# Optimization experiments

Measured on AMD Instinct MI355X. Metric: run time of the kernel, lower is better.

Reference implementation:

```python
import jax, jax.numpy as jnp
import numpy as np

B, D, L, H = 2048, 64, 64, 512  # batch, in_dim, latent_space, hidden


def setup_inputs() -> dict:
    key = jax.random.key(0)
    ks = jax.random.split(key, 12)
    inp = {
        "x": jax.random.normal(ks[0], (B, D), jnp.float32),
        "koopman": jax.random.normal(ks[1], (B, L, D), jnp.float32),
    }
    dims = [(L, H), (H, H), (H, H), (H, D)]
    k = 2
    for pfx in ("s", "t"):
        for j, (fi, fo) in enumerate(dims):
            inp[f"{pfx}W{j+1}"] = jax.random.normal(ks[k], (fi, fo), jnp.float32) / np.sqrt(fi).astype(np.float32)
            inp[f"{pfx}b{j+1}"] = jnp.zeros((fo,), jnp.float32)
            k += 1
    return inp


def _mlp(z, W1, b1, W2, b2, W3, b3, W4, b4):
    h = jnp.tanh(z @ W1 + b1)
    h = jnp.tanh(h @ W2 + b2)
    h = jnp.tanh(h @ W3 + b3)
    return h @ W4 + b4


def reference(x, koopman,
              sW1, sb1, sW2, sb2, sW3, sb3, sW4, sb4,
              tW1, tb1, tW2, tb2, tW3, tb3, tW4, tb4):
    # koopman: (B, L, D) -> z: (B, D, L); column i of the torch loop is z[:, i, :]
    z = jnp.swapaxes(koopman, 1, 2)
    s = _mlp(z, sW1, sb1, sW2, sb2, sW3, sb3, sW4, sb4)  # (B, D, D)
    t = _mlp(z, tW1, tb1, tW2, tb2, tW3, tb3, tW4, tb4)  # (B, D, D)
    # loop kept only output column i for input column i -> diagonal over last two dims
    ds = jnp.diagonal(s, axis1=1, axis2=2)  # (B, D)
    dt = jnp.diagonal(t, axis1=1, axis2=2)  # (B, D)
    return (x - dt) * jnp.exp(-ds)
```

## Files before the change

kernel.cpp:

```cpp
#include <hip/hip_runtime.h>


typedef _Float16 f16;
typedef _Float16 f16x8 __attribute__((ext_vector_type(8)));
typedef float f32x4 __attribute__((ext_vector_type(4)));

#define WPACK_PER_NET 589824
#define OFF_W1 0
#define OFF_W2 32768
#define OFF_W3 294912
#define OFF_W4T 557056
#define WPACK_BYTES (2u * WPACK_PER_NET * sizeof(f16))

__global__ void pack_weights(const float* __restrict__ sW1, const float* __restrict__ sW2,
                             const float* __restrict__ sW3, const float* __restrict__ sW4,
                             const float* __restrict__ tW1, const float* __restrict__ tW2,
                             const float* __restrict__ tW3, const float* __restrict__ tW4,
                             f16* __restrict__ dst) {
  int idx = blockIdx.x * 256 + threadIdx.x;
  if (idx >= 2 * WPACK_PER_NET) return;
  int net = idx >= WPACK_PER_NET;
  int f = idx - net * WPACK_PER_NET;
  const float* W1 = net ? tW1 : sW1;
  const float* W2 = net ? tW2 : sW2;
  const float* W3 = net ? tW3 : sW3;
  const float* W4 = net ? tW4 : sW4;
  float v;
  if (f < OFF_W2) {
    int j = f & 7, lane = (f >> 3) & 63, nt = (f >> 9) & 31, kk = f >> 14;
    v = W1[(kk * 32 + (lane >> 4) * 8 + j) * 512 + nt * 16 + (lane & 15)];
  } else if (f < OFF_W3) {
    int f2 = f - OFF_W2;
    int j = f2 & 7, lane = (f2 >> 3) & 63, nt = (f2 >> 9) & 31, kk = f2 >> 14;
    v = W2[(kk * 32 + (lane >> 4) * 8 + j) * 512 + nt * 16 + (lane & 15)];
  } else if (f < OFF_W4T) {
    int f3 = f - OFF_W3;
    int j = f3 & 7, lane = (f3 >> 3) & 63, nt = (f3 >> 9) & 31, kk = f3 >> 14;
    v = W3[(kk * 32 + (lane >> 4) * 8 + j) * 512 + nt * 16 + (lane & 15)];
  } else {
    int f4 = f - OFF_W4T;
    v = W4[(f4 & 511) * 64 + (f4 >> 9)];
  }
  dst[net * WPACK_PER_NET + f] = (f16)v;
}

__device__ __forceinline__ int aidx(int m, int k) {
  return (((k >> 5) * 4 + (m >> 4)) * 64 + (m & 15) + ((k >> 3) & 3) * 16) * 8 + (k & 7);
}

__device__ __forceinline__ float fast_tanh(float x) {
  float e = __expf(x + x);
  return fmaf(-2.0f, __builtin_amdgcn_rcpf(e + 1.0f), 1.0f);
}

template <bool PACKED>
__device__ __forceinline__ void load_b(const f16* __restrict__ Wblk,
                                       const float* __restrict__ Wraw,
                                       int kk, int wave, int lane, f16x8* bdst) {
  if (PACKED) {
#pragma unroll
    for (int nt = 0; nt < 4; nt++)
      bdst[nt] = *(const f16x8*)(Wblk + kk * 16384 + ((wave * 4 + nt) * 64 + lane) * 8);
  } else {
    int n0 = wave * 64 + (lane & 15);
    int kb = kk * 32 + (lane >> 4) * 8;
#pragma unroll
    for (int nt = 0; nt < 4; nt++) {
      f16x8 v;
#pragma unroll
      for (int j = 0; j < 8; j++) v[j] = (f16)Wraw[(kb + j) * 512 + n0 + nt * 16];
      bdst[nt] = v;
    }
  }
}

template <int NS, bool PACKED>
__device__ __forceinline__ void mlp_layer(const f16* __restrict__ Wblk,
                                          const float* __restrict__ Wraw,
                                          const float* __restrict__ bias,
                                          const f16* Asrc, f16* Hout,
                                          int wave, int lane, int sbase) {
  f32x4 acc[4][4];
#pragma unroll
  for (int nt = 0; nt < 4; nt++) {
    float bv = bias[wave * 64 + nt * 16 + (lane & 15)];
#pragma unroll
    for (int mt = 0; mt < 4; mt++) acc[mt][nt] = f32x4{bv, bv, bv, bv};
  }

  f16x8 bb[2][4];
  load_b<PACKED>(Wblk, Wraw, 0, wave, lane, bb[0]);
#pragma unroll
  for (int kk = 0; kk < NS; kk++) {
    if (kk + 1 < NS) load_b<PACKED>(Wblk, Wraw, kk + 1, wave, lane, bb[(kk + 1) & 1]);
    const f16* ab = Asrc + kk * 2048 + lane * 8;
    f16x8 a[4];
#pragma unroll
    for (int mt = 0; mt < 4; mt++) a[mt] = *(const f16x8*)(ab + mt * 512);
#pragma unroll
    for (int mt = 0; mt < 4; mt++)
#pragma unroll
      for (int nt = 0; nt < 4; nt++)
        acc[mt][nt] = __builtin_amdgcn_mfma_f32_16x16x32_f16(a[mt], bb[kk & 1][nt],
                                                             acc[mt][nt], 0, 0, 0);
  }
  __syncthreads();

  f16* hb = Hout + sbase;
#pragma unroll
  for (int mt = 0; mt < 4; mt++)
#pragma unroll
    for (int nt = 0; nt < 4; nt++)
#pragma unroll
      for (int r = 0; r < 4; r++)
        hb[(nt >> 1) * 2048 + mt * 512 + (nt & 1) * 256 + r * 8] =
            (f16)fast_tanh(acc[mt][nt][r]);
  __syncthreads();
}

template <bool PACKED>
__global__ __launch_bounds__(512, 4) void decoder_main(
    const float* __restrict__ x, const float* __restrict__ koop,
    const f16* __restrict__ wpack,
    const float* __restrict__ sW1, const float* __restrict__ sW2,
    const float* __restrict__ sW3, const float* __restrict__ sW4,
    const float* __restrict__ tW1, const float* __restrict__ tW2,
    const float* __restrict__ tW3, const float* __restrict__ tW4,
    const float* __restrict__ sb1, const float* __restrict__ sb2,
    const float* __restrict__ sb3, const float* __restrict__ sb4,
    const float* __restrict__ tb1, const float* __restrict__ tb2,
    const float* __restrict__ tb3, const float* __restrict__ tb4,
    float* __restrict__ out) {
  __shared__ __align__(16) f16 ZA[4096];
  __shared__ __align__(16) f16 HA[32768];
  __shared__ float redBuf[2][64];

  const int b = blockIdx.x;
  const int t = threadIdx.x;
  const int wave = t >> 6, lane = t & 63;
  const int sbase =
      wave * 4096 + (lane >> 4) * 32 + ((lane & 15) >> 3) * 128 + (lane & 7);

  const float* kb = koop + b * 4096;
#pragma unroll
  for (int i = 0; i < 8; i++) {
    int flat = t + 512 * i;
    ZA[aidx(flat & 63, flat >> 6)] = (f16)kb[flat];
  }
  __syncthreads();

  for (int net = 0; net < 2; net++) {
    const f16* wb = PACKED ? (wpack + net * WPACK_PER_NET) : (const f16*)0;
    const float* W1 = net ? tW1 : sW1;
    const float* W2 = net ? tW2 : sW2;
    const float* W3 = net ? tW3 : sW3;
    const float* W4 = net ? tW4 : sW4;
    const float* b1 = net ? tb1 : sb1;
    const float* b2 = net ? tb2 : sb2;
    const float* b3 = net ? tb3 : sb3;
    const float* b4 = net ? tb4 : sb4;
    mlp_layer<2, PACKED>(PACKED ? wb + OFF_W1 : 0, W1, b1, ZA, HA, wave, lane, sbase);
    mlp_layer<16, PACKED>(PACKED ? wb + OFF_W2 : 0, W2, b2, HA, HA, wave, lane, sbase);
    mlp_layer<16, PACKED>(PACKED ? wb + OFF_W3 : 0, W3, b3, HA, HA, wave, lane, sbase);

    int i = t >> 3, sub = t & 7;
    float p = 0.f;
#pragma unroll
    for (int q = 0; q < 8; q++) {
      int k0 = sub * 64 + q * 8;
      f16x8 hv = *(const f16x8*)&HA[aidx(i, k0)];
      if (PACKED) {
        f16x8 wv = *(const f16x8*)&wb[OFF_W4T + i * 512 + k0];
#pragma unroll
        for (int j = 0; j < 8; j++) p += (float)hv[j] * (float)wv[j];
      } else {
#pragma unroll
        for (int j = 0; j < 8; j++) p += (float)hv[j] * W4[(k0 + j) * 64 + i];
      }
    }
    p += __shfl_down(p, 4, 8);
    p += __shfl_down(p, 2, 8);
    p += __shfl_down(p, 1, 8);
    if (sub == 0) redBuf[net][i] = p + b4[i];
    __syncthreads();
  }

  if (t < 64) {
    out[b * 64 + t] = (x[b * 64 + t] - redBuf[1][t]) * __expf(-redBuf[0][t]);
  }
}

extern "C" void kernel_launch(void* const* d_in, const int* in_sizes, int n_in,
                              void* d_out, int out_size, void* d_ws, size_t ws_size,
                              hipStream_t stream) {
  const float* x    = (const float*)d_in[0];
  const float* koop = (const float*)d_in[1];
  const float* sW1 = (const float*)d_in[2];  const float* sb1 = (const float*)d_in[3];
  const float* sW2 = (const float*)d_in[4];  const float* sb2 = (const float*)d_in[5];
  const float* sW3 = (const float*)d_in[6];  const float* sb3 = (const float*)d_in[7];
  const float* sW4 = (const float*)d_in[8];  const float* sb4 = (const float*)d_in[9];
  const float* tW1 = (const float*)d_in[10]; const float* tb1 = (const float*)d_in[11];
  const float* tW2 = (const float*)d_in[12]; const float* tb2 = (const float*)d_in[13];
  const float* tW3 = (const float*)d_in[14]; const float* tb3 = (const float*)d_in[15];
  const float* tW4 = (const float*)d_in[16]; const float* tb4 = (const float*)d_in[17];
  float* out = (float*)d_out;

  if (ws_size >= (size_t)WPACK_BYTES) {
    f16* wpack = (f16*)d_ws;
    pack_weights<<<4608, 256, 0, stream>>>(sW1, sW2, sW3, sW4, tW1, tW2, tW3, tW4, wpack);
    decoder_main<true><<<2048, 512, 0, stream>>>(
        x, koop, wpack, sW1, sW2, sW3, sW4, tW1, tW2, tW3, tW4,
        sb1, sb2, sb3, sb4, tb1, tb2, tb3, tb4, out);
  } else {
    decoder_main<false><<<2048, 512, 0, stream>>>(
        x, koop, (const f16*)0, sW1, sW2, sW3, sW4, tW1, tW2, tW3, tW4,
        sb1, sb2, sb3, sb4, tb1, tb2, tb3, tb4, out);
  }
}
```

Measured before the change: 435.9 us.

## Split each block's layer work over 16 waves and vectorize weight packing

The main kernel goes from 512 to 1024 threads per block, so each wave computes a 64x32 output tile instead of 64x64. This halves per-wave accumulators and B-fragment loads and is meant to add latency hiding. Separately, the weight packing kernel now has each thread gather 8 values and write one 16-byte vector instead of one scalar. The risk is higher register pressure per block under launch_bounds(1024,4), more barrier cost with 16 waves, and possible loss of occupancy.

```diff
diff --git a/kernel.cpp b/kernel.cpp
--- a/kernel.cpp
+++ b/kernel.cpp
@@ -17,31 +17,39 @@
                              const float* __restrict__ tW1, const float* __restrict__ tW2,
                              const float* __restrict__ tW3, const float* __restrict__ tW4,
                              f16* __restrict__ dst) {
-  int idx = blockIdx.x * 256 + threadIdx.x;
-  if (idx >= 2 * WPACK_PER_NET) return;
-  int net = idx >= WPACK_PER_NET;
-  int f = idx - net * WPACK_PER_NET;
+  int idx8 = (blockIdx.x * 256 + threadIdx.x) * 8;
+  if (idx8 >= 2 * WPACK_PER_NET) return;
+  int net = idx8 >= WPACK_PER_NET;
+  int f = idx8 - net * WPACK_PER_NET;
   const float* W1 = net ? tW1 : sW1;
   const float* W2 = net ? tW2 : sW2;
   const float* W3 = net ? tW3 : sW3;
   const float* W4 = net ? tW4 : sW4;
-  float v;
+  f16x8 o;
   if (f < OFF_W2) {
-    int j = f & 7, lane = (f >> 3) & 63, nt = (f >> 9) & 31, kk = f >> 14;
-    v = W1[(kk * 32 + (lane >> 4) * 8 + j) * 512 + nt * 16 + (lane & 15)];
+    int lane = (f >> 3) & 63, nt = (f >> 9) & 31, kk = f >> 14;
+    int r0 = kk * 32 + (lane >> 4) * 8, c = nt * 16 + (lane & 15);
+#pragma unroll
+    for (int j = 0; j < 8; j++) o[j] = (f16)W1[(r0 + j) * 512 + c];
   } else if (f < OFF_W3) {
     int f2 = f - OFF_W2;
-    int j = f2 & 7, lane = (f2 >> 3) & 63, nt = (f2 >> 9) & 31, kk = f2 >> 14;
-    v = W2[(kk * 32 + (lane >> 4) * 8 + j) * 512 + nt * 16 + (lane & 15)];
+    int lane = (f2 >> 3) & 63, nt = (f2 >> 9) & 31, kk = f2 >> 14;
+    int r0 = kk * 32 + (lane >> 4) * 8, c = nt * 16 + (lane & 15);
+#pragma unroll
+    for (int j = 0; j < 8; j++) o[j] = (f16)W2[(r0 + j) * 512 + c];
   } else if (f < OFF_W4T) {
     int f3 = f - OFF_W3;
-    int j = f3 & 7, lane = (f3 >> 3) & 63, nt = (f3 >> 9) & 31, kk = f3 >> 14;
-    v = W3[(kk * 32 + (lane >> 4) * 8 + j) * 512 + nt * 16 + (lane & 15)];
+    int lane = (f3 >> 3) & 63, nt = (f3 >> 9) & 31, kk = f3 >> 14;
+    int r0 = kk * 32 + (lane >> 4) * 8, c = nt * 16 + (lane & 15);
+#pragma unroll
+    for (int j = 0; j < 8; j++) o[j] = (f16)W3[(r0 + j) * 512 + c];
   } else {
     int f4 = f - OFF_W4T;
-    v = W4[(f4 & 511) * 64 + (f4 >> 9)];
-  }
-  dst[net * WPACK_PER_NET + f] = (f16)v;
+    int i = f4 >> 9, k0 = f4 & 511;
+#pragma unroll
+    for (int j = 0; j < 8; j++) o[j] = (f16)W4[(k0 + j) * 64 + i];
+  }
+  *(f16x8*)(dst + net * WPACK_PER_NET + f) = o;
 }
 
 __device__ __forceinline__ int aidx(int m, int k) {
@@ -59,13 +67,13 @@
                                        int kk, int wave, int lane, f16x8* bdst) {
   if (PACKED) {
 #pragma unroll
-    for (int nt = 0; nt < 4; nt++)
-      bdst[nt] = *(const f16x8*)(Wblk + kk * 16384 + ((wave * 4 + nt) * 64 + lane) * 8);
+    for (int nt = 0; nt < 2; nt++)
+      bdst[nt] = *(const f16x8*)(Wblk + kk * 16384 + ((wave * 2 + nt) * 64 + lane) * 8);
   } else {
-    int n0 = wave * 64 + (lane & 15);
+    int n0 = wave * 32 + (lane & 15);
     int kb = kk * 32 + (lane >> 4) * 8;
 #pragma unroll
-    for (int nt = 0; nt < 4; nt++) {
+    for (int nt = 0; nt < 2; nt++) {
       f16x8 v;
 #pragma unroll
       for (int j = 0; j < 8; j++) v[j] = (f16)Wraw[(kb + j) * 512 + n0 + nt * 16];
@@ -80,15 +88,15 @@
                                           const float* __restrict__ bias,
                                           const f16* Asrc, f16* Hout,
                                           int wave, int lane, int sbase) {
-  f32x4 acc[4][4];
-#pragma unroll
-  for (int nt = 0; nt < 4; nt++) {
-    float bv = bias[wave * 64 + nt * 16 + (lane & 15)];
+  f32x4 acc[4][2];
+#pragma unroll
+  for (int nt = 0; nt < 2; nt++) {
+    float bv = bias[wave * 32 + nt * 16 + (lane & 15)];
 #pragma unroll
     for (int mt = 0; mt < 4; mt++) acc[mt][nt] = f32x4{bv, bv, bv, bv};
   }
 
-  f16x8 bb[2][4];
+  f16x8 bb[2][2];
   load_b<PACKED>(Wblk, Wraw, 0, wave, lane, bb[0]);
 #pragma unroll
   for (int kk = 0; kk < NS; kk++) {
@@ -100,7 +108,7 @@
 #pragma unroll
     for (int mt = 0; mt < 4; mt++)
 #pragma unroll
-      for (int nt = 0; nt < 4; nt++)
+      for (int nt = 0; nt < 2; nt++)
         acc[mt][nt] = __builtin_amdgcn_mfma_f32_16x16x32_f16(a[mt], bb[kk & 1][nt],
                                                              acc[mt][nt], 0, 0, 0);
   }
@@ -110,16 +118,15 @@
 #pragma unroll
   for (int mt = 0; mt < 4; mt++)
 #pragma unroll
-    for (int nt = 0; nt < 4; nt++)
+    for (int nt = 0; nt < 2; nt++)
 #pragma unroll
       for (int r = 0; r < 4; r++)
-        hb[(nt >> 1) * 2048 + mt * 512 + (nt & 1) * 256 + r * 8] =
-            (f16)fast_tanh(acc[mt][nt][r]);
+        hb[mt * 512 + nt * 256 + r * 8] = (f16)fast_tanh(acc[mt][nt][r]);
   __syncthreads();
 }
 
 template <bool PACKED>
-__global__ __launch_bounds__(512, 4) void decoder_main(
+__global__ __launch_bounds__(1024, 4) void decoder_main(
     const float* __restrict__ x, const float* __restrict__ koop,
     const f16* __restrict__ wpack,
     const float* __restrict__ sW1, const float* __restrict__ sW2,
@@ -139,12 +146,12 @@
   const int t = threadIdx.x;
   const int wave = t >> 6, lane = t & 63;
   const int sbase =
-      wave * 4096 + (lane >> 4) * 32 + ((lane & 15) >> 3) * 128 + (lane & 7);
+      wave * 2048 + (lane >> 4) * 32 + ((lane & 15) >> 3) * 128 + (lane & 7);
 
   const float* kb = koop + b * 4096;
 #pragma unroll
-  for (int i = 0; i < 8; i++) {
-    int flat = t + 512 * i;
+  for (int i = 0; i < 4; i++) {
+    int flat = t + 1024 * i;
     ZA[aidx(flat & 63, flat >> 6)] = (f16)kb[flat];
   }
   __syncthreads();
@@ -163,11 +170,11 @@
     mlp_layer<16, PACKED>(PACKED ? wb + OFF_W2 : 0, W2, b2, HA, HA, wave, lane, sbase);
     mlp_layer<16, PACKED>(PACKED ? wb + OFF_W3 : 0, W3, b3, HA, HA, wave, lane, sbase);
 
-    int i = t >> 3, sub = t & 7;
+    int i = t >> 4, sub = t & 15;
     float p = 0.f;
 #pragma unroll
-    for (int q = 0; q < 8; q++) {
-      int k0 = sub * 64 + q * 8;
+    for (int q = 0; q < 4; q++) {
+      int k0 = sub * 32 + q * 8;
       f16x8 hv = *(const f16x8*)&HA[aidx(i, k0)];
       if (PACKED) {
         f16x8 wv = *(const f16x8*)&wb[OFF_W4T + i * 512 + k0];
@@ -178,9 +185,10 @@
         for (int j = 0; j < 8; j++) p += (float)hv[j] * W4[(k0 + j) * 64 + i];
       }
     }
-    p += __shfl_down(p, 4, 8);
-    p += __shfl_down(p, 2, 8);
-    p += __shfl_down(p, 1, 8);
+    p += __shfl_down(p, 8, 16);
+    p += __shfl_down(p, 4, 16);
+    p += __shfl_down(p, 2, 16);
+    p += __shfl_down(p, 1, 16);
     if (sub == 0) redBuf[net][i] = p + b4[i];
     __syncthreads();
   }
@@ -207,12 +215,12 @@
 
   if (ws_size >= (size_t)WPACK_BYTES) {
     f16* wpack = (f16*)d_ws;
-    pack_weights<<<4608, 256, 0, stream>>>(sW1, sW2, sW3, sW4, tW1, tW2, tW3, tW4, wpack);
-    decoder_main<true><<<2048, 512, 0, stream>>>(
+    pack_weights<<<576, 256, 0, stream>>>(sW1, sW2, sW3, sW4, tW1, tW2, tW3, tW4, wpack);
+    decoder_main<true><<<2048, 1024, 0, stream>>>(
         x, koop, wpack, sW1, sW2, sW3, sW4, tW1, tW2, tW3, tW4,
         sb1, sb2, sb3, sb4, tb1, tb2, tb3, tb4, out);
   } else {
-    decoder_main<false><<<2048, 512, 0, stream>>>(
+    decoder_main<false><<<2048, 1024, 0, stream>>>(
         x, koop, (const f16*)0, sW1, sW2, sW3, sW4, tW1, tW2, tW3, tW4,
         sb1, sb2, sb3, sb4, tb1, tb2, tb3, tb4, out);
   }
```

Result: no change. 436.3 us (+0.1%).
